# Optimization experiments

Measured on AMD Instinct MI355X. Metric: run time of the kernel, lower is better.

The kernel has to match this reference:

```python
import jax, jax.numpy as jnp
import numpy as np

B, T, I, H = 64, 512, 512, 512

def setup_inputs() -> dict:
    key = jax.random.key(0)
    ks = jax.random.split(key, 13)
    s = 0.02
    return {
        'inputs': jax.random.normal(ks[0], (B, T, I), dtype=jnp.float32),
        'W_i': jax.random.normal(ks[1], (I, H), dtype=jnp.float32) * s,
        'W_f': jax.random.normal(ks[2], (I, H), dtype=jnp.float32) * s,
        'W_o': jax.random.normal(ks[3], (I, H), dtype=jnp.float32) * s,
        'W_c': jax.random.normal(ks[4], (I, H), dtype=jnp.float32) * s,
        'U_i': jax.random.normal(ks[5], (H, H), dtype=jnp.float32) * s,
        'U_f': jax.random.normal(ks[6], (H, H), dtype=jnp.float32) * s,
        'U_o': jax.random.normal(ks[7], (H, H), dtype=jnp.float32) * s,
        'U_c': jax.random.normal(ks[8], (H, H), dtype=jnp.float32) * s,
        'b_i': jax.random.normal(ks[9], (1, H), dtype=jnp.float32) * s,
        'b_f': jax.random.normal(ks[10], (1, H), dtype=jnp.float32) * s,
        'b_o': jax.random.normal(ks[11], (1, H), dtype=jnp.float32) * s,
        'b_c': jax.random.normal(ks[12], (1, H), dtype=jnp.float32) * s,
    }

def reference(inputs, W_i, W_f, W_o, W_c, U_i, U_f, U_o, U_c, b_i, b_f, b_o, b_c):
    batch = inputs.shape[0]
    hidden = U_i.shape[0]
    # Precompute input projections for all 4 gates in one fused GEMM: [T, B, 4H]
    W = jnp.concatenate([W_i, W_f, W_o, W_c], axis=1)          # [I, 4H]
    b = jnp.concatenate([b_i, b_f, b_o, b_c], axis=1)          # [1, 4H]
    U = jnp.concatenate([U_i, U_f, U_o, U_c], axis=1)          # [H, 4H]
    x_proj = jnp.einsum('bti,ig->tbg', inputs, W) + b          # [T, B, 4H]

    def step(carry, xg):
        h, c = carry
        g = xg + h @ U                                          # [B, 4H]
        i_g = jax.nn.sigmoid(g[:, 0*hidden:1*hidden])
        f_g = jax.nn.sigmoid(g[:, 1*hidden:2*hidden])
        o_g = jax.nn.sigmoid(g[:, 2*hidden:3*hidden])
        c_t = jnp.tanh(g[:, 3*hidden:4*hidden])
        c = f_g * c + i_g * c_t
        h = o_g * jnp.tanh(c)
        return (h, c), None

    h0 = jnp.zeros((batch, hidden), dtype=inputs.dtype)
    c0 = jnp.zeros((batch, hidden), dtype=inputs.dtype)
    (h, c), _ = jax.lax.scan(step, (h0, c0), x_proj)
    return h
```

## Files before the change

### kernel.cpp

```cpp
#include <hip/hip_runtime.h>
#include <hip/hip_bf16.h>
#include <cstdint>


typedef __bf16 bf16;
typedef __bf16 bf16x8 __attribute__((ext_vector_type(8)));
typedef float floatx4 __attribute__((ext_vector_type(4)));
typedef uint64_t u64;
typedef uint32_t u32;

#define T_STEPS 512

#define XP_OFF     0ull
#define XBF_OFF    134217728ull
#define WCT_OFF    167772160ull
#define USW_OFF    169869312ull
#define BCAT_OFF   171966464ull
#define HBUF_OFF   171974656ull

__device__ inline u32 pack_bf16x2(float a, float b) {
    union { __bf16 h[2]; u32 u; } cv;
    cv.h[0] = (__bf16)a; cv.h[1] = (__bf16)b;
    return cv.u;
}
__device__ inline float bf_lo(u32 w) { return __builtin_bit_cast(float, w << 16); }
__device__ inline float bf_hi(u32 w) { return __builtin_bit_cast(float, w & 0xffff0000u); }

__global__ void k0a_convert(const float* __restrict__ in, bf16* __restrict__ xbf) {
    int o = blockIdx.x * 256 + threadIdx.x;
    int k = o & 511;
    int r = o >> 9;
    int t = r >> 6, b = r & 63;
    xbf[o] = (bf16)in[(b * 512 + t) * 512 + k];
}

__global__ void k0b_wcat(const float* __restrict__ Wi, const float* __restrict__ Wf,
                         const float* __restrict__ Wo, const float* __restrict__ Wc,
                         const float* __restrict__ bi, const float* __restrict__ bfv,
                         const float* __restrict__ bo, const float* __restrict__ bc,
                         bf16* __restrict__ wct, float* __restrict__ bcat) {
    int o = blockIdx.x * 256 + threadIdx.x;
    int k = o & 511;
    int c = o >> 9;
    int h = c >> 2, g = c & 3;
    const float* W = (g == 0) ? Wi : (g == 1) ? Wf : (g == 2) ? Wo : Wc;
    wct[o] = (bf16)W[k * 512 + h];
    if (o < 2048) {
        int hh = o >> 2, gg = o & 3;
        const float* bv = (gg == 0) ? bi : (gg == 1) ? bfv : (gg == 2) ? bo : bc;
        bcat[o] = bv[hh];
    }
}

__global__ void k0c_uswz(const float* __restrict__ Ui, const float* __restrict__ Uf,
                         const float* __restrict__ Uo, const float* __restrict__ Uc,
                         bf16* __restrict__ usw) {
    int o = blockIdx.x * 256 + threadIdx.x;
    int e  = o & 7;
    int l  = (o >> 3) & 63;
    int ks = (o >> 9) & 15;
    int nt = (o >> 13) & 1;
    int w  = (o >> 14) & 3;
    int s  = o >> 16;
    int k = ks * 32 + (l >> 4) * 8 + e;
    int col_local = (2 * w + nt) * 16 + (l & 15);
    int h = s * 32 + (col_local >> 2);
    int g = col_local & 3;
    const float* U = (g == 0) ? Ui : (g == 1) ? Uf : (g == 2) ? Uo : Uc;
    usw[o] = (bf16)U[k * 512 + h];
}

__launch_bounds__(256, 2)
__global__ void k1_gemm(const bf16* __restrict__ xbf, const bf16* __restrict__ wct,
                        const float* __restrict__ bcat, bf16* __restrict__ xp) {
    __shared__ bf16 As[128 * 40];
    __shared__ bf16 Bs[128 * 40];
    int tid = threadIdx.x;
    int wid = tid >> 6, lane = tid & 63;
    int q = lane >> 4, m = lane & 15;
    int wr = wid >> 1, wc = wid & 1;
    int br = blockIdx.x & 255, bc = blockIdx.x >> 8;

    floatx4 acc[4][4] = {};

    for (int kk = 0; kk < 16; ++kk) {
        #pragma unroll
        for (int cc = 0; cc < 2; ++cc) {
            int ch = tid + cc * 256;
            int row = ch >> 2, part = ch & 3;
            bf16x8 va = *(const bf16x8*)&xbf[(br * 128 + row) * 512 + kk * 32 + part * 8];
            bf16x8 vb = *(const bf16x8*)&wct[(bc * 128 + row) * 512 + kk * 32 + part * 8];
            *(bf16x8*)&As[row * 40 + part * 8] = va;
            *(bf16x8*)&Bs[row * 40 + part * 8] = vb;
        }
        __syncthreads();
        bf16x8 af[4], bfr[4];
        #pragma unroll
        for (int i = 0; i < 4; ++i) {
            af[i]  = *(const bf16x8*)&As[(wr * 64 + i * 16 + m) * 40 + q * 8];
            bfr[i] = *(const bf16x8*)&Bs[(wc * 64 + i * 16 + m) * 40 + q * 8];
        }
        #pragma unroll
        for (int mt = 0; mt < 4; ++mt)
            #pragma unroll
            for (int nt = 0; nt < 4; ++nt)
                acc[mt][nt] = __builtin_amdgcn_mfma_f32_16x16x32_bf16(
                    af[mt], bfr[nt], acc[mt][nt], 0, 0, 0);
        __syncthreads();
    }
    float bias[4];
    #pragma unroll
    for (int nt = 0; nt < 4; ++nt) bias[nt] = bcat[bc * 128 + wc * 64 + nt * 16 + m];
    #pragma unroll
    for (int mt = 0; mt < 4; ++mt) {
        #pragma unroll
        for (int nt = 0; nt < 4; ++nt) {
            u32 p0 = pack_bf16x2(acc[mt][nt][0] + bias[nt], acc[mt][nt][1] + bias[nt]);
            u32 p1 = pack_bf16x2(acc[mt][nt][2] + bias[nt], acc[mt][nt][3] + bias[nt]);
            size_t idx = (((((size_t)(br * 2 + wr) * 4 + mt) * 16 + bc) * 8
                           + wc * 4 + nt) * 64 + lane) * 4;
            uint2 v; v.x = p0; v.y = p1;
            *(uint2*)&xp[idx] = v;
        }
    }
}

__launch_bounds__(256, 1)
__global__ void k2_rec(const bf16* __restrict__ xp, const bf16* __restrict__ usw,
                       u64* __restrict__ hbuf, float* __restrict__ out) {
    __shared__ bf16 h_lds[16 * 520];
    __shared__ float g_lds[16 * 136];
    u32* h32 = (u32*)h_lds;

    int tid = threadIdx.x;
    int wid = tid >> 6, lane = tid & 63;
    int q = lane >> 4, m = lane & 15;
    int bg = blockIdx.x & 3, s = blockIdx.x >> 2;

    bf16x8 bfr[2][16];
    {
        const bf16x8* base = (const bf16x8*)usw;
        #pragma unroll
        for (int nt = 0; nt < 2; ++nt)
            #pragma unroll
            for (int ks = 0; ks < 16; ++ks)
                bfr[nt][ks] = base[(((s * 4 + wid) * 2 + nt) * 16 + ks) * 64 + lane];
    }

    int r = tid >> 4;
    int jc = (tid & 15) * 2;
    float cs0 = 0.f, cs1 = 0.f;

    for (int t = 0; t < T_STEPS; ++t) {
        floatx4 acc[2];
        {
            size_t b0 = (((((size_t)t * 4 + bg) * 16 + s) * 8 + wid * 2) * 64 + lane) * 4;
            uint2 vx0 = *(const uint2*)&xp[b0];
            uint2 vx1 = *(const uint2*)&xp[b0 + 256];
            acc[0][0] = bf_lo(vx0.x); acc[0][1] = bf_hi(vx0.x);
            acc[0][2] = bf_lo(vx0.y); acc[0][3] = bf_hi(vx0.y);
            acc[1][0] = bf_lo(vx1.x); acc[1][1] = bf_hi(vx1.x);
            acc[1][2] = bf_lo(vx1.y); acc[1][3] = bf_hi(vx1.y);
        }

        if (t > 0) {
            const u64* rb = hbuf + ((size_t)((t - 1) & 1) * 4 + bg) * 4096;
            u32 tg = (u32)t;
            u64 wA[16], wB[16];
            #pragma unroll
            for (int i = 0; i < 16; ++i)
                wA[i] = __hip_atomic_load(rb + tid + 256 * i, __ATOMIC_RELAXED,
                                          __HIP_MEMORY_SCOPE_AGENT);
            #pragma unroll
            for (int i = 0; i < 16; ++i)
                wB[i] = __hip_atomic_load(rb + tid + 256 * i, __ATOMIC_RELAXED,
                                          __HIP_MEMORY_SCOPE_AGENT);
            bool useB = false;
            for (;;) {
                bool ok = true;
                #pragma unroll
                for (int i = 0; i < 16; ++i) ok &= ((u32)(wA[i] >> 32) == tg);
                if (ok) break;
                #pragma unroll
                for (int i = 0; i < 16; ++i)
                    wA[i] = __hip_atomic_load(rb + tid + 256 * i, __ATOMIC_RELAXED,
                                              __HIP_MEMORY_SCOPE_AGENT);
                ok = true;
                #pragma unroll
                for (int i = 0; i < 16; ++i) ok &= ((u32)(wB[i] >> 32) == tg);
                if (ok) { useB = true; break; }
                #pragma unroll
                for (int i = 0; i < 16; ++i)
                    wB[i] = __hip_atomic_load(rb + tid + 256 * i, __ATOMIC_RELAXED,
                                              __HIP_MEMORY_SCOPE_AGENT);
            }
            if (useB) {
                #pragma unroll
                for (int i = 0; i < 16; ++i) wA[i] = wB[i];
            }
            #pragma unroll
            for (int i = 0; i < 16; ++i)
                h32[i * 260 + tid] = (u32)wA[i];
            __syncthreads();
            #pragma unroll
            for (int ks = 0; ks < 16; ++ks) {
                bf16x8 af = *(const bf16x8*)&h_lds[m * 520 + ks * 32 + q * 8];
                acc[0] = __builtin_amdgcn_mfma_f32_16x16x32_bf16(af, bfr[0][ks], acc[0], 0, 0, 0);
                acc[1] = __builtin_amdgcn_mfma_f32_16x16x32_bf16(af, bfr[1][ks], acc[1], 0, 0, 0);
            }
        }

        #pragma unroll
        for (int nt = 0; nt < 2; ++nt) {
            int col = (2 * wid + nt) * 16 + m;
            #pragma unroll
            for (int rr = 0; rr < 4; ++rr)
                g_lds[(q * 4 + rr) * 136 + col] = acc[nt][rr];
        }
        __syncthreads();

        floatx4 ga = *(const floatx4*)&g_lds[r * 136 + jc * 4];
        floatx4 gb = *(const floatx4*)&g_lds[r * 136 + jc * 4 + 4];
        float h0, h1;
        {
            float ig = 1.f / (1.f + __expf(-ga[0]));
            float fg = 1.f / (1.f + __expf(-ga[1]));
            float og = 1.f / (1.f + __expf(-ga[2]));
            float th = 1.f - 2.f / (__expf(2.f * ga[3]) + 1.f);
            cs0 = fg * cs0 + ig * th;
            h0 = og * (1.f - 2.f / (__expf(2.f * cs0) + 1.f));
        }
        {
            float ig = 1.f / (1.f + __expf(-gb[0]));
            float fg = 1.f / (1.f + __expf(-gb[1]));
            float og = 1.f / (1.f + __expf(-gb[2]));
            float th = 1.f - 2.f / (__expf(2.f * gb[3]) + 1.f);
            cs1 = fg * cs1 + ig * th;
            h1 = og * (1.f - 2.f / (__expf(2.f * cs1) + 1.f));
        }
        u64 word = ((u64)(u32)(t + 1) << 32) | (u64)pack_bf16x2(h0, h1);
        __hip_atomic_store(hbuf + (((size_t)(t & 1) * 4 + bg) * 16 + r) * 256
                                + s * 16 + (tid & 15),
                           word, __ATOMIC_RELAXED, __HIP_MEMORY_SCOPE_AGENT);
        if (t == T_STEPS - 1) {
            out[(bg * 16 + r) * 512 + s * 32 + jc]     = h0;
            out[(bg * 16 + r) * 512 + s * 32 + jc + 1] = h1;
        }
    }
}

extern "C" void kernel_launch(void* const* d_in, const int* in_sizes, int n_in,
                              void* d_out, int out_size, void* d_ws, size_t ws_size,
                              hipStream_t stream) {
    const float* inp = (const float*)d_in[0];
    const float* Wi  = (const float*)d_in[1];
    const float* Wf  = (const float*)d_in[2];
    const float* Wo  = (const float*)d_in[3];
    const float* Wc  = (const float*)d_in[4];
    const float* Ui  = (const float*)d_in[5];
    const float* Uf  = (const float*)d_in[6];
    const float* Uo  = (const float*)d_in[7];
    const float* Uc  = (const float*)d_in[8];
    const float* bi  = (const float*)d_in[9];
    const float* bfv = (const float*)d_in[10];
    const float* bo  = (const float*)d_in[11];
    const float* bc  = (const float*)d_in[12];

    char* ws = (char*)d_ws;
    bf16*  xp    = (bf16*)(ws + XP_OFF);
    bf16*  xbf   = (bf16*)(ws + XBF_OFF);
    bf16*  wct   = (bf16*)(ws + WCT_OFF);
    bf16*  usw   = (bf16*)(ws + USW_OFF);
    float* bcat  = (float*)(ws + BCAT_OFF);
    u64*   hbuf  = (u64*)(ws + HBUF_OFF);

    k0a_convert<<<65536, 256, 0, stream>>>(inp, xbf);
    k0b_wcat<<<4096, 256, 0, stream>>>(Wi, Wf, Wo, Wc, bi, bfv, bo, bc, wct, bcat);
    k0c_uswz<<<4096, 256, 0, stream>>>(Ui, Uf, Uo, Uc, usw);
    k1_gemm<<<4096, 256, 0, stream>>>(xbf, wct, bcat, xp);
    k2_rec<<<64, 256, 0, stream>>>(xp, usw, hbuf, (float*)d_out);
}
```

Baseline: 1.589 ms.

## Prefetch next-step x-projection, simplify h polling, use LDS-only barriers

The x-projection load for step t+1 is now issued during step t, so its global-memory latency overlaps the recurrent MFMA work instead of sitting at the head of each step. The double-buffered wA/wB polling of the shared h buffer becomes a single polling buffer. The two __syncthreads calls are replaced by a barrier that waits only on LDS counters (waitcnt 0xc07f) and not on outstanding vector-memory loads, so the in-flight prefetch does not stall the barrier. This shortens the serial per-step critical path, at the cost of relying on hand-coded waitcnt semantics being correct for the LDS traffic.

```diff
diff --git a/kernel.cpp b/kernel.cpp
--- a/kernel.cpp
+++ b/kernel.cpp
@@ -25,6 +25,13 @@
 }
 __device__ inline float bf_lo(u32 w) { return __builtin_bit_cast(float, w << 16); }
 __device__ inline float bf_hi(u32 w) { return __builtin_bit_cast(float, w & 0xffff0000u); }
+
+__device__ inline void lgkm_barrier() {
+    __atomic_signal_fence(__ATOMIC_SEQ_CST);
+    __builtin_amdgcn_s_waitcnt(0xc07f);
+    __builtin_amdgcn_s_barrier();
+    __atomic_signal_fence(__ATOMIC_SEQ_CST);
+}
 
 __global__ void k0a_convert(const float* __restrict__ in, bf16* __restrict__ xbf) {
     int o = blockIdx.x * 256 + threadIdx.x;
@@ -151,63 +158,59 @@
     int jc = (tid & 15) * 2;
     float cs0 = 0.f, cs1 = 0.f;
 
+    uint2 vx0, vx1;
+    {
+        size_t b0 = ((((size_t)bg * 16 + s) * 8 + wid * 2) * 64 + lane) * 4;
+        vx0 = *(const uint2*)&xp[b0];
+        vx1 = *(const uint2*)&xp[b0 + 256];
+    }
+
     for (int t = 0; t < T_STEPS; ++t) {
         floatx4 acc[2];
-        {
-            size_t b0 = (((((size_t)t * 4 + bg) * 16 + s) * 8 + wid * 2) * 64 + lane) * 4;
-            uint2 vx0 = *(const uint2*)&xp[b0];
-            uint2 vx1 = *(const uint2*)&xp[b0 + 256];
+
+        if (t > 0) {
+            const u64* rb = hbuf + ((size_t)((t - 1) & 1) * 4 + bg) * 4096;
+            u32 tg = (u32)t;
+            u64 w[16];
+            #pragma unroll
+            for (int i = 0; i < 16; ++i)
+                w[i] = __hip_atomic_load(rb + tid + 256 * i, __ATOMIC_RELAXED,
+                                         __HIP_MEMORY_SCOPE_AGENT);
             acc[0][0] = bf_lo(vx0.x); acc[0][1] = bf_hi(vx0.x);
             acc[0][2] = bf_lo(vx0.y); acc[0][3] = bf_hi(vx0.y);
             acc[1][0] = bf_lo(vx1.x); acc[1][1] = bf_hi(vx1.x);
             acc[1][2] = bf_lo(vx1.y); acc[1][3] = bf_hi(vx1.y);
-        }
-
-        if (t > 0) {
-            const u64* rb = hbuf + ((size_t)((t - 1) & 1) * 4 + bg) * 4096;
-            u32 tg = (u32)t;
-            u64 wA[16], wB[16];
-            #pragma unroll
-            for (int i = 0; i < 16; ++i)
-                wA[i] = __hip_atomic_load(rb + tid + 256 * i, __ATOMIC_RELAXED,
-                                          __HIP_MEMORY_SCOPE_AGENT);
-            #pragma unroll
-            for (int i = 0; i < 16; ++i)
-                wB[i] = __hip_atomic_load(rb + tid + 256 * i, __ATOMIC_RELAXED,
-                                          __HIP_MEMORY_SCOPE_AGENT);
-            bool useB = false;
             for (;;) {
                 bool ok = true;
                 #pragma unroll
-                for (int i = 0; i < 16; ++i) ok &= ((u32)(wA[i] >> 32) == tg);
+                for (int i = 0; i < 16; ++i) ok &= ((u32)(w[i] >> 32) == tg);
                 if (ok) break;
                 #pragma unroll
                 for (int i = 0; i < 16; ++i)
-                    wA[i] = __hip_atomic_load(rb + tid + 256 * i, __ATOMIC_RELAXED,
-                                              __HIP_MEMORY_SCOPE_AGENT);
-                ok = true;
-                #pragma unroll
-                for (int i = 0; i < 16; ++i) ok &= ((u32)(wB[i] >> 32) == tg);
-                if (ok) { useB = true; break; }
-                #pragma unroll
-                for (int i = 0; i < 16; ++i)
-                    wB[i] = __hip_atomic_load(rb + tid + 256 * i, __ATOMIC_RELAXED,
-                                              __HIP_MEMORY_SCOPE_AGENT);
+                    w[i] = __hip_atomic_load(rb + tid + 256 * i, __ATOMIC_RELAXED,
+                                             __HIP_MEMORY_SCOPE_AGENT);
             }
-            if (useB) {
-                #pragma unroll
-                for (int i = 0; i < 16; ++i) wA[i] = wB[i];
-            }
             #pragma unroll
             for (int i = 0; i < 16; ++i)
-                h32[i * 260 + tid] = (u32)wA[i];
-            __syncthreads();
+                h32[i * 260 + tid] = (u32)w[i];
+            lgkm_barrier();
             #pragma unroll
             for (int ks = 0; ks < 16; ++ks) {
                 bf16x8 af = *(const bf16x8*)&h_lds[m * 520 + ks * 32 + q * 8];
                 acc[0] = __builtin_amdgcn_mfma_f32_16x16x32_bf16(af, bfr[0][ks], acc[0], 0, 0, 0);
                 acc[1] = __builtin_amdgcn_mfma_f32_16x16x32_bf16(af, bfr[1][ks], acc[1], 0, 0, 0);
             }
+        } else {
+            acc[0][0] = bf_lo(vx0.x); acc[0][1] = bf_hi(vx0.x);
+            acc[0][2] = bf_lo(vx0.y); acc[0][3] = bf_hi(vx0.y);
+            acc[1][0] = bf_lo(vx1.x); acc[1][1] = bf_hi(vx1.x);
+            acc[1][2] = bf_lo(vx1.y); acc[1][3] = bf_hi(vx1.y);
+        }
+
+        if (t + 1 < T_STEPS) {
+            size_t b0 = (((((size_t)(t + 1) * 4 + bg) * 16 + s) * 8 + wid * 2) * 64 + lane) * 4;
+            vx0 = *(const uint2*)&xp[b0];
+            vx1 = *(const uint2*)&xp[b0 + 256];
         }
 
         #pragma unroll
@@ -217,7 +220,7 @@
             for (int rr = 0; rr < 4; ++rr)
                 g_lds[(q * 4 + rr) * 136 + col] = acc[nt][rr];
         }
-        __syncthreads();
+        lgkm_barrier();
 
         floatx4 ga = *(const floatx4*)&g_lds[r * 136 + jc * 4];
         floatx4 gb = *(const floatx4*)&g_lds[r * 136 + jc * 4 + 4];
```

After: 1.612 ms. About the same (+1.4%).
